# Performance work log

Measured on AMD Instinct MI355X. Metric: run time of the kernel, lower is better.

Reference implementation:

```python
import jax, jax.numpy as jnp
import numpy as np

N_NODES = 50000
N_EDGES = 400000
IN_NODE = 16
OUT_NODE = 20
IN_EDGE = 10
HIDDEN_EDGE = 64
HIDDEN_ACTOR = 256
N_ACTIONS = 16
N_GRAPHS = 128
BN_EPS = 1e-5


def setup_inputs() -> dict:
    key = jax.random.key(0)
    ks = jax.random.split(key, 16)
    inp = {
        "x": jax.random.normal(ks[0], (N_NODES, IN_NODE), dtype=jnp.float32),
        "edge_index": jax.random.randint(ks[1], (2, N_EDGES), 0, N_NODES, dtype=jnp.int64),
        "edge_attr": jax.random.normal(ks[2], (N_EDGES, IN_EDGE), dtype=jnp.float32),
        "batch": jnp.sort(jax.random.randint(ks[3], (N_NODES,), 0, N_GRAPHS, dtype=jnp.int64)),
        # edge-nn params: Lin(in_edge,64) -> BN(64) -> ReLU -> Lin(64, in*out)
        "W1": jax.random.normal(ks[4], (IN_EDGE, HIDDEN_EDGE), dtype=jnp.float32) / np.sqrt(IN_EDGE),
        "b1": jnp.zeros((HIDDEN_EDGE,), dtype=jnp.float32),
        "gamma": jnp.ones((HIDDEN_EDGE,), dtype=jnp.float32),
        "beta": jnp.zeros((HIDDEN_EDGE,), dtype=jnp.float32),
        "W2": jax.random.normal(ks[5], (HIDDEN_EDGE, IN_NODE * OUT_NODE), dtype=jnp.float32) / np.sqrt(HIDDEN_EDGE),
        "b2": jnp.zeros((IN_NODE * OUT_NODE,), dtype=jnp.float32),
        # NNConv root weight + bias
        "root": jax.random.normal(ks[6], (IN_NODE, OUT_NODE), dtype=jnp.float32) / np.sqrt(IN_NODE),
        "bias": jnp.zeros((OUT_NODE,), dtype=jnp.float32),
        # actor MLP: Lin(20,256) -> ReLU -> Lin(256, n_actions)
        "A1": jax.random.normal(ks[7], (OUT_NODE, HIDDEN_ACTOR), dtype=jnp.float32) / np.sqrt(OUT_NODE),
        "ab1": jnp.zeros((HIDDEN_ACTOR,), dtype=jnp.float32),
        "A2": jax.random.normal(ks[8], (HIDDEN_ACTOR, N_ACTIONS), dtype=jnp.float32) / np.sqrt(HIDDEN_ACTOR),
        "ab2": jnp.zeros((N_ACTIONS,), dtype=jnp.float32),
    }
    return inp


def reference(x, edge_index, edge_attr, batch, W1, b1, gamma, beta, W2, b2, root, bias, A1, ab1, A2, ab2):
    # edge nn: Linear -> BatchNorm1d (training-mode batch stats) -> ReLU -> Linear
    h = edge_attr @ W1 + b1                                  # [E, 64]
    mu = jnp.mean(h, axis=0)
    var = jnp.mean((h - mu) ** 2, axis=0)                    # biased var, as BN uses
    h = gamma * (h - mu) * jax.lax.rsqrt(var + BN_EPS) + beta
    h = jax.nn.relu(h)
    w = (h @ W2 + b2).reshape(-1, IN_NODE, OUT_NODE)         # [E, in, out]

    src, dst = edge_index[0], edge_index[1]
    msg = jnp.einsum('ei,eio->eo', x[src], w)                # per-edge matvec, [E, out]
    agg = jax.ops.segment_sum(msg, dst, num_segments=N_NODES)  # scatter-add to targets
    out = agg + x @ root + bias                              # [N, out]

    # global_mean_pool over graphs
    sums = jax.ops.segment_sum(out, batch, num_segments=N_GRAPHS)
    counts = jax.ops.segment_sum(jnp.ones((out.shape[0],), out.dtype), batch, num_segments=N_GRAPHS)
    pooled = sums / jnp.maximum(counts, 1.0)[:, None]        # [G, out]

    a = jax.nn.relu(pooled @ A1 + ab1)
    return a @ A2 + ab2                                      # [G, n_actions]
```

## Files before the change

### kernel.cpp

```cpp
#include <hip/hip_runtime.h>

#define N_NODES   50000
#define N_EDGES   400000
#define IN_NODE   16
#define OUT_NODE  20
#define IN_EDGE   10
#define HE        64
#define HA        256
#define N_ACT     16
#define N_GRAPHS  128
#define BN_EPS    1e-5f
#define HNST      68
#define SPLIT     16
#define NB        1563
#define NCH       25
#define GB        256
#define XB        196

typedef __attribute__((ext_vector_type(8))) short short8v;
typedef __attribute__((ext_vector_type(4))) float f32x4;

__device__ __forceinline__ unsigned short f2bf(float f) {
  unsigned u = __float_as_uint(f);
  u += 0x7fffu + ((u >> 16) & 1u);
  return (unsigned short)(u >> 16);
}
__device__ __forceinline__ float bf2f(short s) {
  return __uint_as_float(((unsigned)(unsigned short)s) << 16);
}

#define DPP_ROR_ADD(v, CTRL)                                                  \
  ((v) + __int_as_float(__builtin_amdgcn_update_dpp(                          \
             0, __float_as_int(v), (CTRL), 0xF, 0xF, true)))
#define ROW_SUM16(v)                                                          \
  do {                                                                        \
    v = DPP_ROR_ADD(v, 0x128);                                                \
    v = DPP_ROR_ADD(v, 0x124);                                                \
    v = DPP_ROR_ADD(v, 0x122);                                                \
    v = DPP_ROR_ADD(v, 0x121);                                                \
  } while (0)

__global__ void zero_k(float* __restrict__ ws) {
  ws[blockIdx.x * 256 + threadIdx.x] = 0.f;
}

__global__ __launch_bounds__(256) void gramcount_k(
    const float* __restrict__ ea, const int* __restrict__ ei,
    const int* __restrict__ batch, float* __restrict__ hdr,
    int* __restrict__ ge, int* __restrict__ cnt2dT) {
  __shared__ float red[4][72];
  __shared__ int lh[N_GRAPHS];
  const int tid = threadIdx.x;

  if (blockIdx.x < GB) {
    float cs[10];
    float gm[55];
#pragma unroll
    for (int a = 0; a < 10; ++a) cs[a] = 0.f;
#pragma unroll
    for (int u = 0; u < 55; ++u) gm[u] = 0.f;

    for (int e = blockIdx.x * 256 + tid; e < N_EDGES; e += GB * 256) {
      const float2* rp = reinterpret_cast<const float2*>(ea + (size_t)e * 10);
      float f[10];
#pragma unroll
      for (int p = 0; p < 5; ++p) {
        const float2 t = rp[p];
        f[2 * p] = t.x;
        f[2 * p + 1] = t.y;
      }
#pragma unroll
      for (int a = 0; a < 10; ++a) cs[a] += f[a];
      int idx = 0;
#pragma unroll
      for (int a = 0; a < 10; ++a)
#pragma unroll
        for (int b = a; b < 10; ++b) {
          gm[idx] = fmaf(f[a], f[b], gm[idx]);
          ++idx;
        }
    }

#pragma unroll
    for (int v = 0; v < 10; ++v)
#pragma unroll
      for (int off = 1; off < 64; off <<= 1)
        cs[v] += __shfl_xor(cs[v], off, 64);
#pragma unroll
    for (int u = 0; u < 55; ++u)
#pragma unroll
      for (int off = 1; off < 64; off <<= 1)
        gm[u] += __shfl_xor(gm[u], off, 64);

    const int lane = tid & 63;
    const int w = tid >> 6;
    if (lane == 0) {
#pragma unroll
      for (int v = 0; v < 10; ++v) red[w][v] = cs[v];
#pragma unroll
      for (int u = 0; u < 55; ++u) red[w][10 + u] = gm[u];
    }
    __syncthreads();
    if (tid < 65) {
      const float s = red[0][tid] + red[1][tid] + red[2][tid] + red[3][tid];
      const int dst = (tid < 10) ? tid : 6 + tid;
      atomicAdd(&hdr[dst], s);
    }
    return;
  }

  const int b = blockIdx.x - GB;
  const int e = b * 256 + tid;
  if (tid < N_GRAPHS) lh[tid] = 0;
  __syncthreads();
  if (e < N_EDGES) {
    const int g = batch[ei[N_EDGES + e]];
    ge[e] = g;
    atomicAdd(&lh[g], 1);
  }
  __syncthreads();
  if (tid < N_GRAPHS) cnt2dT[tid * NB + b] = lh[tid];
}

__global__ __launch_bounds__(128) void colscanfin_k(
    const int* __restrict__ cnt2dT, int* __restrict__ off2dT,
    int* __restrict__ hist, const float* __restrict__ hdr,
    const float* __restrict__ W1, const float* __restrict__ b1,
    const float* __restrict__ gamma, const float* __restrict__ beta,
    float* __restrict__ scale, float* __restrict__ c1out) {
  const int t = threadIdx.x;
  if (blockIdx.x < N_GRAPHS) {
    if (t >= 64) return;
    const int g = blockIdx.x;
    int vals[NCH];
#pragma unroll
    for (int c = 0; c < NCH; ++c) {
      const int b = c * 64 + t;
      vals[c] = (b < NB) ? cnt2dT[g * NB + b] : 0;
    }
    int running = 0;
#pragma unroll
    for (int c = 0; c < NCH; ++c) {
      int s = vals[c];
#pragma unroll
      for (int off = 1; off < 64; off <<= 1) {
        const int y = __shfl_up(s, off, 64);
        if (t >= off) s += y;
      }
      const int b = c * 64 + t;
      if (b < NB) off2dT[g * NB + b] = running + s - vals[c];
      running += __shfl(s, 63, 64);
    }
    if (t == 0) hist[g] = running;
    return;
  }

  if (t < HE) {
    const int c = t;
    float wc[10];
#pragma unroll
    for (int k = 0; k < 10; ++k) wc[k] = W1[k * HE + c];
    float su = 0.f;
#pragma unroll
    for (int k = 0; k < 10; ++k) su = fmaf(hdr[k], wc[k], su);
    float q = 0.f;
    int idx = 0;
#pragma unroll
    for (int a = 0; a < 10; ++a) {
      q = fmaf(hdr[16 + idx], wc[a] * wc[a], q);
      ++idx;
#pragma unroll
      for (int b = a + 1; b < 10; ++b) {
        q = fmaf(2.f * hdr[16 + idx], wc[a] * wc[b], q);
        ++idx;
      }
    }
    const float b1c = b1[c];
    const float invE = 1.f / (float)N_EDGES;
    const float mu = su * invE + b1c;
    const float Eh2 = (q + 2.f * b1c * su) * invE + b1c * b1c;
    const float var = Eh2 - mu * mu;
    const float sc = gamma[c] * rsqrtf(var + BN_EPS);
    scale[c] = sc;
    c1out[c] = sc * (b1c - mu) + beta[c];
  }
}

__global__ void scan_k(const int* __restrict__ hist,
                       int* __restrict__ bstart) {
  __shared__ int v[N_GRAPHS];
  const int t = threadIdx.x;
  const int h = hist[t];
  v[t] = h;
  __syncthreads();
  for (int off = 1; off < N_GRAPHS; off <<= 1) {
    int y = 0;
    if (t >= off) y = v[t - off];
    __syncthreads();
    v[t] += y;
    __syncthreads();
  }
  bstart[t] = v[t] - h;
  if (t == N_GRAPHS - 1) bstart[N_GRAPHS] = v[t];
}

__global__ __launch_bounds__(256) void scatxsum_k(
    const float* __restrict__ ea, const int* __restrict__ ei,
    const int* __restrict__ ge, const float* __restrict__ x,
    const int* __restrict__ off2dT, const int* __restrict__ bstart,
    unsigned short* __restrict__ exb, const int* __restrict__ batch,
    float* __restrict__ XN, float* __restrict__ cnt) {
  const int tid = threadIdx.x;
  if (blockIdx.x < NB) {
    __shared__ int lh[N_GRAPHS];
    __shared__ int obase[N_GRAPHS];
    const int b = blockIdx.x;
    const int e = b * 256 + tid;
    if (tid < N_GRAPHS) lh[tid] = 0;
    __syncthreads();
    int g = -1, r = 0;
    if (e < N_EDGES) {
      g = ge[e];
      r = atomicAdd(&lh[g], 1);
    }
    if (tid < N_GRAPHS) obase[tid] = bstart[tid] + off2dT[tid * NB + b];
    __syncthreads();
    if (e >= N_EDGES) return;

    const float2* rp = reinterpret_cast<const float2*>(ea + (size_t)e * 10);
    float f[10];
#pragma unroll
    for (int p = 0; p < 5; ++p) {
      const float2 t2 = rp[p];
      f[2 * p] = t2.x;
      f[2 * p + 1] = t2.y;
    }
    const int s = ei[e];
    const float4* xp = reinterpret_cast<const float4*>(&x[(size_t)s * IN_NODE]);
    const float4 x0 = xp[0], x1 = xp[1], x2 = xp[2], x3 = xp[3];

    unsigned u[16];
    u[0] = f2bf(f[0]) | ((unsigned)f2bf(f[1]) << 16);
    u[1] = f2bf(f[2]) | ((unsigned)f2bf(f[3]) << 16);
    u[2] = f2bf(f[4]) | ((unsigned)f2bf(f[5]) << 16);
    u[3] = f2bf(f[6]) | ((unsigned)f2bf(f[7]) << 16);
    u[4] = f2bf(f[8]) | ((unsigned)f2bf(f[9]) << 16);
    u[5] = 0; u[6] = 0; u[7] = 0;
    u[8]  = f2bf(x0.x) | ((unsigned)f2bf(x0.y) << 16);
    u[9]  = f2bf(x0.z) | ((unsigned)f2bf(x0.w) << 16);
    u[10] = f2bf(x1.x) | ((unsigned)f2bf(x1.y) << 16);
    u[11] = f2bf(x1.z) | ((unsigned)f2bf(x1.w) << 16);
    u[12] = f2bf(x2.x) | ((unsigned)f2bf(x2.y) << 16);
    u[13] = f2bf(x2.z) | ((unsigned)f2bf(x2.w) << 16);
    u[14] = f2bf(x3.x) | ((unsigned)f2bf(x3.y) << 16);
    u[15] = f2bf(x3.z) | ((unsigned)f2bf(x3.w) << 16);

    const int pos = obase[g] + r;
    int4* dst = reinterpret_cast<int4*>(exb + (size_t)pos * 32);
    dst[0] = int4{(int)u[0], (int)u[1], (int)u[2], (int)u[3]};
    dst[1] = int4{(int)u[4], (int)u[5], (int)u[6], (int)u[7]};
    dst[2] = int4{(int)u[8], (int)u[9], (int)u[10], (int)u[11]};
    dst[3] = int4{(int)u[12], (int)u[13], (int)u[14], (int)u[15]};
    return;
  }

  __shared__ float xn_l[N_GRAPHS * IN_NODE];
  __shared__ float cnt_l[N_GRAPHS];
  const int lane = tid & 63;
  for (int t = tid; t < N_GRAPHS * IN_NODE; t += 256) xn_l[t] = 0.f;
  if (tid < N_GRAPHS) cnt_l[tid] = 0.f;
  __syncthreads();

  const int n = (blockIdx.x - NB) * 256 + tid;
  const bool valid = n < N_NODES;
  int g = -1;
  float xf[IN_NODE];
  if (valid) {
    g = batch[n];
    const float4* xp = reinterpret_cast<const float4*>(&x[(size_t)n * IN_NODE]);
    const float4 a0 = xp[0], a1 = xp[1], a2 = xp[2], a3 = xp[3];
    xf[0] = a0.x;  xf[1] = a0.y;  xf[2] = a0.z;  xf[3] = a0.w;
    xf[4] = a1.x;  xf[5] = a1.y;  xf[6] = a1.z;  xf[7] = a1.w;
    xf[8] = a2.x;  xf[9] = a2.y;  xf[10] = a2.z; xf[11] = a2.w;
    xf[12] = a3.x; xf[13] = a3.y; xf[14] = a3.z; xf[15] = a3.w;
  } else {
#pragma unroll
    for (int i = 0; i < IN_NODE; ++i) xf[i] = 0.f;
  }

  const int g0 = __builtin_amdgcn_readfirstlane(g);
  const bool uni = (__ballot(valid && (g == g0)) == 0xFFFFFFFFFFFFFFFFull);

  if (uni) {
#pragma unroll
    for (int i = 0; i < IN_NODE; ++i) {
      float s = xf[i];
      ROW_SUM16(s);
      s += __shfl_xor(s, 16, 64);
      s += __shfl_xor(s, 32, 64);
      xf[i] = s;
    }
    if (lane == 0) {
#pragma unroll
      for (int i = 0; i < IN_NODE; ++i)
        atomicAdd(&xn_l[g0 * IN_NODE + i], xf[i]);
      atomicAdd(&cnt_l[g0], 64.f);
    }
  } else if (valid) {
#pragma unroll
    for (int i = 0; i < IN_NODE; ++i) atomicAdd(&xn_l[g * IN_NODE + i], xf[i]);
    atomicAdd(&cnt_l[g], 1.f);
  }
  __syncthreads();

  if (tid < N_GRAPHS && cnt_l[tid] != 0.f) atomicAdd(&cnt[tid], cnt_l[tid]);
  for (int t = tid; t < N_GRAPHS * IN_NODE; t += 256) {
    const float v = xn_l[t];
    if (v != 0.f) atomicAdd(&XN[t], v);
  }
}

__global__ __launch_bounds__(256, 4) void s_kernel(
    const unsigned short* __restrict__ exb, const float* __restrict__ W1g,
    const float* __restrict__ scale, const float* __restrict__ c1g,
    const int* __restrict__ bstart, float* __restrict__ Spart,
    float* __restrict__ XSpart) {
  __shared__ short hnT[2][64 * HNST];
  __shared__ short xT[2][16 * HNST];
  __shared__ float scs[HE], c1s[HE];

  const int tid = threadIdx.x;
  const int lane = tid & 63;
  const int w = tid >> 6;
  const int i_col = lane & 15;
  const int kq = lane >> 4;

  if (tid < HE) {
    scs[tid] = scale[tid];
    c1s[tid] = c1g[tid];
  }
  __syncthreads();

  const int g = blockIdx.x / SPLIT;
  const int pp = blockIdx.x - g * SPLIT;
  const int gs = bstart[g], geE = bstart[g + 1];
  const int cnt = geE - gs;
  const int p0 = gs + (cnt * pp) / SPLIT;
  const int p1 = gs + (cnt * (pp + 1)) / SPLIT;

  short8v w1f[4];
  float scv[4], c1v[4];
#pragma unroll
  for (int nt = 0; nt < 4; ++nt) {
    short8v v;
#pragma unroll
    for (int j = 0; j < 8; ++j) {
      const int k = kq * 8 + j;
      const float f = (k < IN_EDGE) ? W1g[k * HE + nt * 16 + i_col] : 0.f;
      v[j] = (short)f2bf(f);
    }
    w1f[nt] = v;
    scv[nt] = scs[nt * 16 + i_col];
    c1v[nt] = c1s[nt * 16 + i_col];
  }

  f32x4 acc = {0.f, 0.f, 0.f, 0.f};
  float xs = 0.f;

  int p = 0;
  for (int base = p0; base < p1; base += 64) {
    {
      const int er = base + w * 16 + i_col;
      short8v ae;
      if (kq < 2) {
        ae = *reinterpret_cast<const short8v*>(&exb[(size_t)er * 32 + kq * 8]);
      } else {
#pragma unroll
        for (int j = 0; j < 8; ++j) ae[j] = 0;
      }
      const f32x4 zero4 = {0.f, 0.f, 0.f, 0.f};
#pragma unroll
      for (int nt = 0; nt < 4; ++nt) {
        const f32x4 hv = __builtin_amdgcn_mfma_f32_16x16x32_bf16(
            ae, w1f[nt], zero4, 0, 0, 0);
        short4 sv;
        {
          const int e0 = base + w * 16 + kq * 4;
          const float h0 = (e0 + 0 < p1) ? fmaxf(fmaf(hv[0], scv[nt], c1v[nt]), 0.f) : 0.f;
          const float h1 = (e0 + 1 < p1) ? fmaxf(fmaf(hv[1], scv[nt], c1v[nt]), 0.f) : 0.f;
          const float h2 = (e0 + 2 < p1) ? fmaxf(fmaf(hv[2], scv[nt], c1v[nt]), 0.f) : 0.f;
          const float h3 = (e0 + 3 < p1) ? fmaxf(fmaf(hv[3], scv[nt], c1v[nt]), 0.f) : 0.f;
          sv.x = (short)f2bf(h0);
          sv.y = (short)f2bf(h1);
          sv.z = (short)f2bf(h2);
          sv.w = (short)f2bf(h3);
        }
        *reinterpret_cast<short4*>(
            &hnT[p][(nt * 16 + i_col) * HNST + w * 16 + kq * 4]) = sv;
      }
    }
    {
      const int et = tid >> 2, iq = tid & 3;
      const int er = base + et;
      short4 xv = {0, 0, 0, 0};
      if (er < p1)
        xv = *reinterpret_cast<const short4*>(
            &exb[(size_t)er * 32 + 16 + iq * 4]);
      xT[p][(iq * 4 + 0) * HNST + et] = xv.x;
      xT[p][(iq * 4 + 1) * HNST + et] = xv.y;
      xT[p][(iq * 4 + 2) * HNST + et] = xv.z;
      xT[p][(iq * 4 + 3) * HNST + et] = xv.w;
    }
    __syncthreads();
#pragma unroll
    for (int ks = 0; ks < 2; ++ks) {
      const short8v a = *reinterpret_cast<const short8v*>(
          &hnT[p][(w * 16 + i_col) * HNST + ks * 32 + kq * 8]);
      const short8v b = *reinterpret_cast<const short8v*>(
          &xT[p][i_col * HNST + ks * 32 + kq * 8]);
      acc = __builtin_amdgcn_mfma_f32_16x16x32_bf16(a, b, acc, 0, 0, 0);
      if (w == 0) {
#pragma unroll
        for (int j = 0; j < 8; ++j) xs += bf2f(b[j]);
      }
    }
    p ^= 1;
  }

#pragma unroll
  for (int r = 0; r < 4; ++r)
    Spart[(size_t)blockIdx.x * 1024 + (w * 16 + kq * 4 + r) * 16 + i_col] =
        acc[r];
  if (w == 0) {
    xs += __shfl_xor(xs, 16, 64);
    xs += __shfl_xor(xs, 32, 64);
    if (kq == 0) XSpart[blockIdx.x * 16 + i_col] = xs;
  }
}

__global__ __launch_bounds__(256) void fuse_k(
    const float* __restrict__ Spart, const float* __restrict__ XSpart,
    const float* __restrict__ W2g, const float* __restrict__ b2g,
    const float* __restrict__ XN, const float* __restrict__ cnt,
    const float* __restrict__ rootg, const float* __restrict__ biasg,
    const float* __restrict__ A1, const float* __restrict__ ab1,
    const float* __restrict__ A2, const float* __restrict__ ab2,
    float* __restrict__ out) {
  __shared__ float S_l[1024];
  __shared__ float xs_l[16];
  __shared__ float xn_f[16];
  __shared__ float pooled[OUT_NODE];
  __shared__ float a_s[HA];
  __shared__ float red[16][N_ACT];

  const int g = blockIdx.x;
  const int tid = threadIdx.x, lane = tid & 63, w = tid >> 6;

  for (int t = tid; t < 1024; t += 256) {
    float s = 0.f;
#pragma unroll
    for (int q = 0; q < SPLIT; ++q)
      s += Spart[(size_t)(SPLIT * g + q) * 1024 + t];
    S_l[t] = s;
  }
  if (tid < 16) {
    float s = 0.f;
#pragma unroll
    for (int q = 0; q < SPLIT; ++q) s += XSpart[(SPLIT * g + q) * 16 + tid];
    xs_l[tid] = s;
    xn_f[tid] = XN[g * IN_NODE + tid];
  }
  __syncthreads();

  const float invc = 1.f / fmaxf(cnt[g], 1.f);
#pragma unroll
  for (int oi = 0; oi < 5; ++oi) {
    const int o = w * 5 + oi;
    float s = 0.f;
#pragma unroll
    for (int j = 0; j < 16; ++j) {
      const int u = lane + 64 * j;
      const int c = u >> 4, i = u & 15;
      s = fmaf(S_l[u], W2g[c * (IN_NODE * OUT_NODE) + i * OUT_NODE + o], s);
    }
    if (lane < 16) {
      s = fmaf(xs_l[lane], b2g[lane * OUT_NODE + o], s);
      s = fmaf(xn_f[lane], rootg[lane * OUT_NODE + o], s);
    }
    ROW_SUM16(s);
    s += __shfl_xor(s, 16, 64);
    s += __shfl_xor(s, 32, 64);
    if (lane == 0) pooled[o] = s * invc + biasg[o];
  }
  __syncthreads();

  {
    float v = ab1[tid];
#pragma unroll
    for (int k = 0; k < OUT_NODE; ++k)
      v = fmaf(pooled[k], A1[k * HA + tid], v);
    a_s[tid] = fmaxf(v, 0.f);
  }
  __syncthreads();
  {
    const int j = tid & 15, seg = tid >> 4;
    float v = 0.f;
#pragma unroll
    for (int kk = 0; kk < 16; ++kk) {
      const int k = seg * 16 + kk;
      v += a_s[k] * A2[k * N_ACT + j];
    }
    red[seg][j] = v;
  }
  __syncthreads();
  if (tid < N_ACT) {
    float s = ab2[tid];
#pragma unroll
    for (int seg = 0; seg < 16; ++seg) s += red[seg][tid];
    out[g * N_ACT + tid] = s;
  }
}

extern "C" void kernel_launch(void* const* d_in, const int* in_sizes, int n_in,
                              void* d_out, int out_size, void* d_ws,
                              size_t ws_size, hipStream_t stream) {
  const float* x     = (const float*)d_in[0];
  const int*   ei    = (const int*)d_in[1];
  const float* ea    = (const float*)d_in[2];
  const int*   batch = (const int*)d_in[3];
  const float* W1    = (const float*)d_in[4];
  const float* b1    = (const float*)d_in[5];
  const float* gamma = (const float*)d_in[6];
  const float* beta  = (const float*)d_in[7];
  const float* W2    = (const float*)d_in[8];
  const float* b2    = (const float*)d_in[9];
  const float* root  = (const float*)d_in[10];
  const float* bias  = (const float*)d_in[11];
  const float* A1    = (const float*)d_in[12];
  const float* ab1   = (const float*)d_in[13];
  const float* A2    = (const float*)d_in[14];
  const float* ab2   = (const float*)d_in[15];
  float* out = (float*)d_out;

  float* ws = (float*)d_ws;
  int*   iw = (int*)d_ws;
  float* hdr     = ws;
  float* scale   = ws + 128;
  float* c1      = ws + 192;
  float* XN      = ws + 256;
  float* cntb    = ws + 2304;
  int*   bstart  = iw + 2560;
  int*   hist    = iw + 2704;
  int*   cnt2dT  = iw + 2848;
  int*   off2dT  = iw + 202912;
  float* Spart   = ws + 402976;
  float* XSpart  = ws + 2500128;
  unsigned short* exb = (unsigned short*)(iw + 2532896);
  int*   ge      = iw + 402976;

  zero_k<<<10, 256, 0, stream>>>(ws);
  gramcount_k<<<GB + NB, 256, 0, stream>>>(ea, ei, batch, hdr, ge, cnt2dT);
  colscanfin_k<<<N_GRAPHS + 1, 128, 0, stream>>>(cnt2dT, off2dT, hist, hdr,
                                                 W1, b1, gamma, beta, scale,
                                                 c1);
  scan_k<<<1, 128, 0, stream>>>(hist, bstart);
  scatxsum_k<<<NB + XB, 256, 0, stream>>>(ea, ei, ge, x, off2dT, bstart, exb,
                                          batch, XN, cntb);
  s_kernel<<<N_GRAPHS * SPLIT, 256, 0, stream>>>(exb, W1, scale, c1, bstart,
                                                 Spart, XSpart);
  fuse_k<<<N_GRAPHS, 256, 0, stream>>>(Spart, XSpart, W2, b2, XN, cntb, root,
                                       bias, A1, ab1, A2, ab2, out);
}
```

Before: 83.97 us.

## Drop scan kernel by recomputing graph prefix sums per block; halve edge blocks

Removes the single-block scan_k launch and instead has every scatter block and every s_kernel block recompute the 128-entry exclusive prefix sum of the graph histogram in shared memory. The edge-count and scatter kernels now handle two edges per thread, strided by SEG2, which halves the number of per-block histogram columns (NB) and the work of the column scan (NCH). The aim is to cut one kernel launch and dependency bubble and to shrink the 2D count table, in exchange for redundant scan work and extra barriers in every block.

```diff
diff --git a/kernel.cpp b/kernel.cpp
--- a/kernel.cpp
+++ b/kernel.cpp
@@ -12,8 +12,9 @@
 #define BN_EPS    1e-5f
 #define HNST      68
 #define SPLIT     16
-#define NB        1563
-#define NCH       25
+#define NB        782
+#define SEG2      200192
+#define NCH       13
 #define GB        256
 #define XB        196
 
@@ -110,13 +111,16 @@
   }
 
   const int b = blockIdx.x - GB;
-  const int e = b * 256 + tid;
   if (tid < N_GRAPHS) lh[tid] = 0;
   __syncthreads();
-  if (e < N_EDGES) {
-    const int g = batch[ei[N_EDGES + e]];
-    ge[e] = g;
-    atomicAdd(&lh[g], 1);
+#pragma unroll
+  for (int j = 0; j < 2; ++j) {
+    const int e = b * 256 + tid + j * SEG2;
+    if (e < N_EDGES) {
+      const int g = batch[ei[N_EDGES + e]];
+      ge[e] = g;
+      atomicAdd(&lh[g], 1);
+    }
   }
   __syncthreads();
   if (tid < N_GRAPHS) cnt2dT[tid * NB + b] = lh[tid];
@@ -186,81 +190,89 @@
   }
 }
 
-__global__ void scan_k(const int* __restrict__ hist,
-                       int* __restrict__ bstart) {
-  __shared__ int v[N_GRAPHS];
-  const int t = threadIdx.x;
-  const int h = hist[t];
-  v[t] = h;
-  __syncthreads();
-  for (int off = 1; off < N_GRAPHS; off <<= 1) {
-    int y = 0;
-    if (t >= off) y = v[t - off];
-    __syncthreads();
-    v[t] += y;
-    __syncthreads();
-  }
-  bstart[t] = v[t] - h;
-  if (t == N_GRAPHS - 1) bstart[N_GRAPHS] = v[t];
-}
-
 __global__ __launch_bounds__(256) void scatxsum_k(
     const float* __restrict__ ea, const int* __restrict__ ei,
     const int* __restrict__ ge, const float* __restrict__ x,
-    const int* __restrict__ off2dT, const int* __restrict__ bstart,
+    const int* __restrict__ off2dT, const int* __restrict__ hist,
     unsigned short* __restrict__ exb, const int* __restrict__ batch,
     float* __restrict__ XN, float* __restrict__ cnt) {
   const int tid = threadIdx.x;
   if (blockIdx.x < NB) {
     __shared__ int lh[N_GRAPHS];
+    __shared__ int vtmp[N_GRAPHS];
     __shared__ int obase[N_GRAPHS];
     const int b = blockIdx.x;
-    const int e = b * 256 + tid;
-    if (tid < N_GRAPHS) lh[tid] = 0;
-    __syncthreads();
-    int g = -1, r = 0;
-    if (e < N_EDGES) {
-      g = ge[e];
-      r = atomicAdd(&lh[g], 1);
-    }
-    if (tid < N_GRAPHS) obase[tid] = bstart[tid] + off2dT[tid * NB + b];
-    __syncthreads();
-    if (e >= N_EDGES) return;
-
-    const float2* rp = reinterpret_cast<const float2*>(ea + (size_t)e * 10);
-    float f[10];
-#pragma unroll
-    for (int p = 0; p < 5; ++p) {
-      const float2 t2 = rp[p];
-      f[2 * p] = t2.x;
-      f[2 * p + 1] = t2.y;
-    }
-    const int s = ei[e];
-    const float4* xp = reinterpret_cast<const float4*>(&x[(size_t)s * IN_NODE]);
-    const float4 x0 = xp[0], x1 = xp[1], x2 = xp[2], x3 = xp[3];
-
-    unsigned u[16];
-    u[0] = f2bf(f[0]) | ((unsigned)f2bf(f[1]) << 16);
-    u[1] = f2bf(f[2]) | ((unsigned)f2bf(f[3]) << 16);
-    u[2] = f2bf(f[4]) | ((unsigned)f2bf(f[5]) << 16);
-    u[3] = f2bf(f[6]) | ((unsigned)f2bf(f[7]) << 16);
-    u[4] = f2bf(f[8]) | ((unsigned)f2bf(f[9]) << 16);
-    u[5] = 0; u[6] = 0; u[7] = 0;
-    u[8]  = f2bf(x0.x) | ((unsigned)f2bf(x0.y) << 16);
-    u[9]  = f2bf(x0.z) | ((unsigned)f2bf(x0.w) << 16);
-    u[10] = f2bf(x1.x) | ((unsigned)f2bf(x1.y) << 16);
-    u[11] = f2bf(x1.z) | ((unsigned)f2bf(x1.w) << 16);
-    u[12] = f2bf(x2.x) | ((unsigned)f2bf(x2.y) << 16);
-    u[13] = f2bf(x2.z) | ((unsigned)f2bf(x2.w) << 16);
-    u[14] = f2bf(x3.x) | ((unsigned)f2bf(x3.y) << 16);
-    u[15] = f2bf(x3.z) | ((unsigned)f2bf(x3.w) << 16);
-
-    const int pos = obase[g] + r;
-    int4* dst = reinterpret_cast<int4*>(exb + (size_t)pos * 32);
-    dst[0] = int4{(int)u[0], (int)u[1], (int)u[2], (int)u[3]};
-    dst[1] = int4{(int)u[4], (int)u[5], (int)u[6], (int)u[7]};
-    dst[2] = int4{(int)u[8], (int)u[9], (int)u[10], (int)u[11]};
-    dst[3] = int4{(int)u[12], (int)u[13], (int)u[14], (int)u[15]};
+    const int h = (tid < N_GRAPHS) ? hist[tid] : 0;
+    if (tid < N_GRAPHS) {
+      vtmp[tid] = h;
+      lh[tid] = 0;
+    }
+    __syncthreads();
+    for (int off = 1; off < N_GRAPHS; off <<= 1) {
+      int y = 0;
+      if (tid < N_GRAPHS && tid >= off) y = vtmp[tid - off];
+      __syncthreads();
+      if (tid < N_GRAPHS) vtmp[tid] += y;
+      __syncthreads();
+    }
+    if (tid < N_GRAPHS)
+      obase[tid] = (vtmp[tid] - h) + off2dT[tid * NB + b];
+    __syncthreads();
+
+    int gj[2], lr[2];
+#pragma unroll
+    for (int j = 0; j < 2; ++j) {
+      const int e = b * 256 + tid + j * SEG2;
+      gj[j] = -1;
+      lr[j] = 0;
+      if (e < N_EDGES) {
+        const int g = ge[e];
+        gj[j] = g;
+        lr[j] = atomicAdd(&lh[g], 1);
+      }
+    }
+    __syncthreads();
+
+#pragma unroll
+    for (int j = 0; j < 2; ++j) {
+      if (gj[j] < 0) continue;
+      const int e = b * 256 + tid + j * SEG2;
+      const float2* rp = reinterpret_cast<const float2*>(ea + (size_t)e * 10);
+      float f[10];
+#pragma unroll
+      for (int p = 0; p < 5; ++p) {
+        const float2 t2 = rp[p];
+        f[2 * p] = t2.x;
+        f[2 * p + 1] = t2.y;
+      }
+      const int s = ei[e];
+      const float4* xp =
+          reinterpret_cast<const float4*>(&x[(size_t)s * IN_NODE]);
+      const float4 x0 = xp[0], x1 = xp[1], x2 = xp[2], x3 = xp[3];
+
+      unsigned u[16];
+      u[0] = f2bf(f[0]) | ((unsigned)f2bf(f[1]) << 16);
+      u[1] = f2bf(f[2]) | ((unsigned)f2bf(f[3]) << 16);
+      u[2] = f2bf(f[4]) | ((unsigned)f2bf(f[5]) << 16);
+      u[3] = f2bf(f[6]) | ((unsigned)f2bf(f[7]) << 16);
+      u[4] = f2bf(f[8]) | ((unsigned)f2bf(f[9]) << 16);
+      u[5] = 0; u[6] = 0; u[7] = 0;
+      u[8]  = f2bf(x0.x) | ((unsigned)f2bf(x0.y) << 16);
+      u[9]  = f2bf(x0.z) | ((unsigned)f2bf(x0.w) << 16);
+      u[10] = f2bf(x1.x) | ((unsigned)f2bf(x1.y) << 16);
+      u[11] = f2bf(x1.z) | ((unsigned)f2bf(x1.w) << 16);
+      u[12] = f2bf(x2.x) | ((unsigned)f2bf(x2.y) << 16);
+      u[13] = f2bf(x2.z) | ((unsigned)f2bf(x2.w) << 16);
+      u[14] = f2bf(x3.x) | ((unsigned)f2bf(x3.y) << 16);
+      u[15] = f2bf(x3.z) | ((unsigned)f2bf(x3.w) << 16);
+
+      const int pos = obase[gj[j]] + lr[j];
+      int4* dst = reinterpret_cast<int4*>(exb + (size_t)pos * 32);
+      dst[0] = int4{(int)u[0], (int)u[1], (int)u[2], (int)u[3]};
+      dst[1] = int4{(int)u[4], (int)u[5], (int)u[6], (int)u[7]};
+      dst[2] = int4{(int)u[8], (int)u[9], (int)u[10], (int)u[11]};
+      dst[3] = int4{(int)u[12], (int)u[13], (int)u[14], (int)u[15]};
+    }
     return;
   }
 
@@ -323,11 +335,13 @@
 __global__ __launch_bounds__(256, 4) void s_kernel(
     const unsigned short* __restrict__ exb, const float* __restrict__ W1g,
     const float* __restrict__ scale, const float* __restrict__ c1g,
-    const int* __restrict__ bstart, float* __restrict__ Spart,
+    const int* __restrict__ hist, float* __restrict__ Spart,
     float* __restrict__ XSpart) {
   __shared__ short hnT[2][64 * HNST];
   __shared__ short xT[2][16 * HNST];
   __shared__ float scs[HE], c1s[HE];
+  __shared__ int vtmp[N_GRAPHS];
+  __shared__ int sb[N_GRAPHS + 1];
 
   const int tid = threadIdx.x;
   const int lane = tid & 63;
@@ -339,11 +353,25 @@
     scs[tid] = scale[tid];
     c1s[tid] = c1g[tid];
   }
+  const int h = (tid < N_GRAPHS) ? hist[tid] : 0;
+  if (tid < N_GRAPHS) vtmp[tid] = h;
+  __syncthreads();
+  for (int off = 1; off < N_GRAPHS; off <<= 1) {
+    int y = 0;
+    if (tid < N_GRAPHS && tid >= off) y = vtmp[tid - off];
+    __syncthreads();
+    if (tid < N_GRAPHS) vtmp[tid] += y;
+    __syncthreads();
+  }
+  if (tid < N_GRAPHS) {
+    sb[tid] = vtmp[tid] - h;
+    if (tid == N_GRAPHS - 1) sb[N_GRAPHS] = vtmp[tid];
+  }
   __syncthreads();
 
   const int g = blockIdx.x / SPLIT;
   const int pp = blockIdx.x - g * SPLIT;
-  const int gs = bstart[g], geE = bstart[g + 1];
+  const int gs = sb[g], geE = sb[g + 1];
   const int cnt = geE - gs;
   const int p0 = gs + (cnt * pp) / SPLIT;
   const int p1 = gs + (cnt * (pp + 1)) / SPLIT;
@@ -549,7 +577,6 @@
   float* c1      = ws + 192;
   float* XN      = ws + 256;
   float* cntb    = ws + 2304;
-  int*   bstart  = iw + 2560;
   int*   hist    = iw + 2704;
   int*   cnt2dT  = iw + 2848;
   int*   off2dT  = iw + 202912;
@@ -563,10 +590,9 @@
   colscanfin_k<<<N_GRAPHS + 1, 128, 0, stream>>>(cnt2dT, off2dT, hist, hdr,
                                                  W1, b1, gamma, beta, scale,
                                                  c1);
-  scan_k<<<1, 128, 0, stream>>>(hist, bstart);
-  scatxsum_k<<<NB + XB, 256, 0, stream>>>(ea, ei, ge, x, off2dT, bstart, exb,
+  scatxsum_k<<<NB + XB, 256, 0, stream>>>(ea, ei, ge, x, off2dT, hist, exb,
                                           batch, XN, cntb);
-  s_kernel<<<N_GRAPHS * SPLIT, 256, 0, stream>>>(exb, W1, scale, c1, bstart,
+  s_kernel<<<N_GRAPHS * SPLIT, 256, 0, stream>>>(exb, W1, scale, c1, hist,
                                                  Spart, XSpart);
   fuse_k<<<N_GRAPHS, 256, 0, stream>>>(Spart, XSpart, W2, b2, XN, cntb, root,
                                        bias, A1, ab1, A2, ab2, out);
```

Measured after the change: 81.17 us. 3.3% less time.
